# Kernel tuning notes

Hardware: AMD Instinct MI355X
Metric: run time of the kernel (lower is better)

The kernel has to match this reference:

```python
import jax, jax.numpy as jnp
import numpy as np

B = 32768      # batch
D = 512        # embedding dim
V = 100000     # vocab_length (row 0 reserved -> table has V+1 rows)
S = 100        # num_neg_samples (hard-coded in source)
DISTORTION = 0.4


def _expected_counts():
    # fixed_unigram sampler: zipf-ish counts, distorted by 0.4, 1 reserved id
    counts = 1.0 / np.arange(1, V + 1, dtype=np.float64)
    p = counts ** DISTORTION
    p = p / p.sum()
    q = np.zeros(V + 1, dtype=np.float64)
    # unique sampling expected count: E[id in sample] = 1-(1-p)^S
    q[1:] = -np.expm1(S * np.log1p(-p))
    q[0] = 1e-9  # reserved id, never sampled; avoid log(0)
    return q


def setup_inputs() -> dict:
    key = jax.random.key(0)
    k1, k2, k3, k4 = jax.random.split(key, 4)
    label = jax.random.randint(k1, (B,), 1, V + 1, dtype=jnp.int64)
    inputs = jax.random.normal(k2, (B, D), dtype=jnp.float32)
    weights = jax.random.normal(k3, (V + 1, D), dtype=jnp.float32) * 0.05
    biases = jnp.zeros((V + 1,), dtype=jnp.float32)
    sampled_ids = jax.random.choice(k4, V, (S,), replace=False).astype(jnp.int64) + 1
    q = jnp.asarray(_expected_counts(), dtype=jnp.float32)
    true_expected_count = q[label]          # [B]
    sampled_expected_count = q[sampled_ids]  # [S]
    return {
        "label": label, "inputs": inputs, "weights": weights, "biases": biases,
        "sampled_ids": sampled_ids,
        "true_expected_count": true_expected_count,
        "sampled_expected_count": sampled_expected_count,
    }


def reference(label, inputs, weights, biases, sampled_ids,
              true_expected_count, sampled_expected_count):
    # --- _compute_sampled_logits with subtract_log_q=True ---
    true_w = weights[label]                                   # [B, D] gather
    true_logits = (jnp.einsum('bd,bd->b', inputs, true_w)
                   + biases[label]
                   - jnp.log(true_expected_count))            # [B]
    samp_w = weights[sampled_ids]                             # [S, D] gather
    samp_logits = (jnp.einsum('bd,sd->bs', inputs, samp_w)
                   + biases[sampled_ids]
                   - jnp.log(sampled_expected_count))         # [B, S]
    logits = jnp.concatenate([true_logits[:, None], samp_logits], axis=1)  # [B, 1+S]
    # labels are one-hot at column 0 -> CE = logsumexp - true logit
    losses = jax.nn.logsumexp(logits, axis=1) - logits[:, 0]
    loss = jnp.mean(losses)
    return logits, loss
```

## Files before the change

kernel.cpp:

```cpp
#include <hip/hip_runtime.h>
#include <math.h>

#define B_TOT 32768
#define DIM   512
#define NS    100
#define NCOL  101
#define TB    128
#define NBLK  (B_TOT / TB)

#define BASE_OFF 28672
#define LPART_OFF 28800
#define NPACK (16 * 7 * 64)

typedef __attribute__((ext_vector_type(8))) short short8;
typedef __attribute__((ext_vector_type(4))) float f32x4;

static __device__ __forceinline__ short f2bf(float f) {
    unsigned u = __builtin_bit_cast(unsigned, f);
    unsigned r = (u + 0x7FFFu + ((u >> 16) & 1u)) >> 16;
    return (short)r;
}

__global__ __launch_bounds__(256)
void pack_kernel(const float* __restrict__ weights, const float* __restrict__ biases,
                 const int* __restrict__ sids, const float* __restrict__ sq,
                 short* __restrict__ wpack, float* __restrict__ base_g)
{
    const int tid = blockIdx.x * 256 + threadIdx.x;
    if (tid < 112)
        base_g[tid] = (tid < NS) ? biases[sids[tid]] - logf(sq[tid]) : -INFINITY;
    if (tid >= NPACK) return;
    const int kc = tid / 448, rem = tid % 448;
    const int c = rem >> 6, l = rem & 63;
    const int col = c * 16 + (l & 15);
    const int k   = kc * 32 + (l >> 4) * 8;
    short8 v = (short8){0, 0, 0, 0, 0, 0, 0, 0};
    if (col < NS) {
        const float* src = weights + (long)sids[col] * DIM + k;
        const float4 f0 = *(const float4*)src;
        const float4 f1 = *(const float4*)(src + 4);
        v[0] = f2bf(f0.x); v[1] = f2bf(f0.y); v[2] = f2bf(f0.z); v[3] = f2bf(f0.w);
        v[4] = f2bf(f1.x); v[5] = f2bf(f1.y); v[6] = f2bf(f1.z); v[7] = f2bf(f1.w);
    }
    *(short8*)&wpack[(long)tid * 8] = v;
}

__global__ __launch_bounds__(512, 4)
void fused_kernel(const int* __restrict__ label,
                  const float* __restrict__ inputs,
                  const float* __restrict__ weights,
                  const float* __restrict__ biases,
                  const float* __restrict__ tq,
                  const short* __restrict__ wpack,
                  const float* __restrict__ base_g,
                  float* __restrict__ out,
                  float* __restrict__ lpart)
{
    const int t    = threadIdx.x;
    const int wave = t >> 6;
    const int lane = t & 63;
    const int rit  = lane & 15;
    const int seg  = lane >> 4;
    const int absRow = blockIdx.x * TB + wave * 16 + rit;
    const int lab = label[absRow];
    const float* aptr = inputs  + (long)absRow * DIM + seg * 8;
    const float* wtp  = weights + (long)lab    * DIM + seg * 8;

    float base_v[7];
    #pragma unroll
    for (int c = 0; c < 7; c++) base_v[c] = base_g[c * 16 + rit];

    f32x4 acc[7];
    #pragma unroll
    for (int c = 0; c < 7; c++) acc[c] = (f32x4){0.f, 0.f, 0.f, 0.f};
    float tacc = 0.f;

    #pragma unroll
    for (int kc = 0; kc < DIM / 32; kc++) {
        const int k0 = kc * 32;
        const float4 a0 = *(const float4*)(aptr + k0);
        const float4 a1 = *(const float4*)(aptr + k0 + 4);
        const float4 w0 = *(const float4*)(wtp + k0);
        const float4 w1 = *(const float4*)(wtp + k0 + 4);

        tacc = fmaf(a0.x, w0.x, tacc); tacc = fmaf(a0.y, w0.y, tacc);
        tacc = fmaf(a0.z, w0.z, tacc); tacc = fmaf(a0.w, w0.w, tacc);
        tacc = fmaf(a1.x, w1.x, tacc); tacc = fmaf(a1.y, w1.y, tacc);
        tacc = fmaf(a1.z, w1.z, tacc); tacc = fmaf(a1.w, w1.w, tacc);

        short8 af;
        af[0] = f2bf(a0.x); af[1] = f2bf(a0.y); af[2] = f2bf(a0.z); af[3] = f2bf(a0.w);
        af[4] = f2bf(a1.x); af[5] = f2bf(a1.y); af[6] = f2bf(a1.z); af[7] = f2bf(a1.w);

        const short* wp = wpack + ((long)kc * 7 * 64 + lane) * 8;
        #pragma unroll
        for (int c = 0; c < 7; c++) {
            const short8 bf = *(const short8*)(wp + c * 64 * 8);
            acc[c] = __builtin_amdgcn_mfma_f32_16x16x32_bf16(af, bf, acc[c], 0, 0, 0);
        }
    }

    tacc += __shfl_xor(tacc, 16);
    tacc += __shfl_xor(tacc, 32);
    const float tl = tacc + biases[lab] - logf(tq[absRow]);
    if (lane < 16) out[(long)absRow * NCOL] = tl;

    const int g = lane >> 4;
    float loss_sum = 0.f;
    #pragma unroll
    for (int i = 0; i < 4; i++) {
        const int r = g * 4 + i;
        const long orow = (long)(blockIdx.x * TB + wave * 16 + r) * NCOL;
        const float tlv = __shfl(tl, r);
        float v[7];
        float m = tlv;
        #pragma unroll
        for (int c = 0; c < 7; c++) {
            v[c] = acc[c][i] + base_v[c];
            m = fmaxf(m, v[c]);
        }
        #pragma unroll
        for (int off = 1; off < 16; off <<= 1) m = fmaxf(m, __shfl_xor(m, off));
        float s = (rit == 0) ? expf(tlv - m) : 0.f;
        #pragma unroll
        for (int c = 0; c < 7; c++) s += expf(v[c] - m);
        #pragma unroll
        for (int off = 1; off < 16; off <<= 1) s += __shfl_xor(s, off);
        loss_sum += m + logf(s) - tlv;
        #pragma unroll
        for (int c = 0; c < 7; c++) {
            const int col = c * 16 + rit;
            if (col < NS) out[orow + 1 + col] = v[c];
        }
    }
    float wl = (rit == 0) ? loss_sum : 0.f;
    wl += __shfl_xor(wl, 16);
    wl += __shfl_xor(wl, 32);
    if (lane == 0) lpart[blockIdx.x * 8 + wave] = wl;
}

__global__ __launch_bounds__(256)
void reduce_kernel(const float* __restrict__ lpart, float* __restrict__ out_loss)
{
    double s = 0.0;
    for (int i = threadIdx.x; i < NBLK * 8; i += 256) s += (double)lpart[i];
    __shared__ double buf[256];
    buf[threadIdx.x] = s;
    __syncthreads();
    for (int o = 128; o > 0; o >>= 1) {
        if (threadIdx.x < o) buf[threadIdx.x] += buf[threadIdx.x + o];
        __syncthreads();
    }
    if (threadIdx.x == 0) *out_loss = (float)(buf[0] * (1.0 / (double)B_TOT));
}

extern "C" void kernel_launch(void* const* d_in, const int* in_sizes, int n_in,
                              void* d_out, int out_size, void* d_ws, size_t ws_size,
                              hipStream_t stream)
{
    const int*   label   = (const int*)d_in[0];
    const float* inputs  = (const float*)d_in[1];
    const float* weights = (const float*)d_in[2];
    const float* biases  = (const float*)d_in[3];
    const int*   sids    = (const int*)d_in[4];
    const float* tq      = (const float*)d_in[5];
    const float* sq      = (const float*)d_in[6];
    float* out  = (float*)d_out;
    float* ws_f = (float*)d_ws;
    short* wpack  = (short*)d_ws;
    float* base_g = ws_f + BASE_OFF;
    float* lpart  = ws_f + LPART_OFF;

    pack_kernel<<<28, 256, 0, stream>>>(weights, biases, sids, sq, wpack, base_g);
    fused_kernel<<<NBLK, 512, 0, stream>>>(label, inputs, weights, biases, tq,
                                           wpack, base_g, out, lpart);
    reduce_kernel<<<1, 256, 0, stream>>>(lpart, out + (long)B_TOT * NCOL);
}
```

Before: 44.02 us.

## Stage packed weights in LDS and split K across wave pairs

The fused kernel now launches 1024 threads per block. It copies the whole bf16 packed sample-weight matrix (about 112 KB) into LDS once per block, and pairs of waves each handle half of the K dimension for the same 16 rows. Their partial MFMA accumulators and true-logit dot products are combined through LDS before the softmax/loss epilogue. The aim is to cut repeated global/L2 reads of the packed weights and double the wave parallelism per row tile. In exchange, the large LDS footprint likely limits residency to one block per CU, and the change adds extra barriers and an LDS reduction step. The per-block loss is also pre-summed, so the reduce kernel reads only 256 values.

New measurement: 41.40 us. -5.9%, faster.

```diff
diff --git a/kernel.cpp b/kernel.cpp
--- a/kernel.cpp
+++ b/kernel.cpp
@@ -7,10 +7,10 @@
 #define NCOL  101
 #define TB    128
 #define NBLK  (B_TOT / TB)
+#define NPACK (16 * 7 * 64)
 
 #define BASE_OFF 28672
 #define LPART_OFF 28800
-#define NPACK (16 * 7 * 64)
 
 typedef __attribute__((ext_vector_type(8))) short short8;
 typedef __attribute__((ext_vector_type(4))) float f32x4;
@@ -45,7 +45,7 @@
     *(short8*)&wpack[(long)tid * 8] = v;
 }
 
-__global__ __launch_bounds__(512, 4)
+__global__ __launch_bounds__(1024, 4)
 void fused_kernel(const int* __restrict__ label,
                   const float* __restrict__ inputs,
                   const float* __restrict__ weights,
@@ -56,27 +56,40 @@
                   float* __restrict__ out,
                   float* __restrict__ lpart)
 {
-    const int t    = threadIdx.x;
+    __shared__ short W_lds[NPACK * 8];
+    __shared__ float tl_x[TB];
+    __shared__ float ls_lds[8];
+
+    const int t = threadIdx.x;
+
+    {
+        const short8* src = (const short8*)wpack;
+        short8* dst = (short8*)W_lds;
+        #pragma unroll
+        for (int s = 0; s < 7; s++)
+            dst[s * 1024 + t] = src[s * 1024 + t];
+    }
+
     const int wave = t >> 6;
     const int lane = t & 63;
+    const int rg   = wave >> 1;
+    const int kh   = wave & 1;
     const int rit  = lane & 15;
     const int seg  = lane >> 4;
-    const int absRow = blockIdx.x * TB + wave * 16 + rit;
+    const int absRow = blockIdx.x * TB + rg * 16 + rit;
     const int lab = label[absRow];
-    const float* aptr = inputs  + (long)absRow * DIM + seg * 8;
-    const float* wtp  = weights + (long)lab    * DIM + seg * 8;
-
-    float base_v[7];
-    #pragma unroll
-    for (int c = 0; c < 7; c++) base_v[c] = base_g[c * 16 + rit];
+    const float* aptr = inputs  + (long)absRow * DIM + kh * 256 + seg * 8;
+    const float* wtp  = weights + (long)lab    * DIM + kh * 256 + seg * 8;
 
     f32x4 acc[7];
     #pragma unroll
     for (int c = 0; c < 7; c++) acc[c] = (f32x4){0.f, 0.f, 0.f, 0.f};
     float tacc = 0.f;
 
+    __syncthreads();
+
     #pragma unroll
-    for (int kc = 0; kc < DIM / 32; kc++) {
+    for (int kc = 0; kc < 8; kc++) {
         const int k0 = kc * 32;
         const float4 a0 = *(const float4*)(aptr + k0);
         const float4 a1 = *(const float4*)(aptr + k0 + 4);
@@ -92,7 +105,8 @@
         af[0] = f2bf(a0.x); af[1] = f2bf(a0.y); af[2] = f2bf(a0.z); af[3] = f2bf(a0.w);
         af[4] = f2bf(a1.x); af[5] = f2bf(a1.y); af[6] = f2bf(a1.z); af[7] = f2bf(a1.w);
 
-        const short* wp = wpack + ((long)kc * 7 * 64 + lane) * 8;
+        const int kcg = kh * 8 + kc;
+        const short* wp = &W_lds[((kcg * 7) * 64 + lane) * 8];
         #pragma unroll
         for (int c = 0; c < 7; c++) {
             const short8 bf = *(const short8*)(wp + c * 64 * 8);
@@ -102,50 +116,84 @@
 
     tacc += __shfl_xor(tacc, 16);
     tacc += __shfl_xor(tacc, 32);
-    const float tl = tacc + biases[lab] - logf(tq[absRow]);
-    if (lane < 16) out[(long)absRow * NCOL] = tl;
-
-    const int g = lane >> 4;
-    float loss_sum = 0.f;
-    #pragma unroll
-    for (int i = 0; i < 4; i++) {
-        const int r = g * 4 + i;
-        const long orow = (long)(blockIdx.x * TB + wave * 16 + r) * NCOL;
-        const float tlv = __shfl(tl, r);
-        float v[7];
-        float m = tlv;
-        #pragma unroll
-        for (int c = 0; c < 7; c++) {
-            v[c] = acc[c][i] + base_v[c];
-            m = fmaxf(m, v[c]);
+
+    __syncthreads();
+
+    float* ex = (float*)W_lds;
+    if (kh == 1) {
+        const int base = rg * 1856 + lane * 29;
+        #pragma unroll
+        for (int c = 0; c < 7; c++)
+            #pragma unroll
+            for (int i = 0; i < 4; i++)
+                ex[base + c * 4 + i] = acc[c][i];
+        if (lane < 16) tl_x[rg * 16 + lane] = tacc;
+    }
+    __syncthreads();
+
+    if (kh == 0) {
+        const int base = rg * 1856 + lane * 29;
+        #pragma unroll
+        for (int c = 0; c < 7; c++)
+            #pragma unroll
+            for (int i = 0; i < 4; i++)
+                acc[c][i] += ex[base + c * 4 + i];
+        tacc += tl_x[rg * 16 + rit];
+
+        float base_v[7];
+        #pragma unroll
+        for (int c = 0; c < 7; c++) base_v[c] = base_g[c * 16 + rit];
+
+        const float tl = tacc + biases[lab] - logf(tq[absRow]);
+        if (lane < 16) out[(long)absRow * NCOL] = tl;
+
+        const int g = lane >> 4;
+        float loss_sum = 0.f;
+        #pragma unroll
+        for (int i = 0; i < 4; i++) {
+            const int r = g * 4 + i;
+            const long orow = (long)(blockIdx.x * TB + rg * 16 + r) * NCOL;
+            const float tlv = __shfl(tl, r);
+            float v[7];
+            float m = tlv;
+            #pragma unroll
+            for (int c = 0; c < 7; c++) {
+                v[c] = acc[c][i] + base_v[c];
+                m = fmaxf(m, v[c]);
+            }
+            #pragma unroll
+            for (int off = 1; off < 16; off <<= 1) m = fmaxf(m, __shfl_xor(m, off));
+            float s = (rit == 0) ? expf(tlv - m) : 0.f;
+            #pragma unroll
+            for (int c = 0; c < 7; c++) s += expf(v[c] - m);
+            #pragma unroll
+            for (int off = 1; off < 16; off <<= 1) s += __shfl_xor(s, off);
+            loss_sum += m + logf(s) - tlv;
+            #pragma unroll
+            for (int c = 0; c < 7; c++) {
+                const int col = c * 16 + rit;
+                if (col < NS) out[orow + 1 + col] = v[c];
+            }
         }
-        #pragma unroll
-        for (int off = 1; off < 16; off <<= 1) m = fmaxf(m, __shfl_xor(m, off));
-        float s = (rit == 0) ? expf(tlv - m) : 0.f;
-        #pragma unroll
-        for (int c = 0; c < 7; c++) s += expf(v[c] - m);
-        #pragma unroll
-        for (int off = 1; off < 16; off <<= 1) s += __shfl_xor(s, off);
-        loss_sum += m + logf(s) - tlv;
-        #pragma unroll
-        for (int c = 0; c < 7; c++) {
-            const int col = c * 16 + rit;
-            if (col < NS) out[orow + 1 + col] = v[c];
-        }
-    }
-    float wl = (rit == 0) ? loss_sum : 0.f;
-    wl += __shfl_xor(wl, 16);
-    wl += __shfl_xor(wl, 32);
-    if (lane == 0) lpart[blockIdx.x * 8 + wave] = wl;
+        float wl = (rit == 0) ? loss_sum : 0.f;
+        wl += __shfl_xor(wl, 16);
+        wl += __shfl_xor(wl, 32);
+        if (lane == 0) ls_lds[rg] = wl;
+    }
+    __syncthreads();
+    if (t == 0) {
+        float bp = 0.f;
+        #pragma unroll
+        for (int w = 0; w < 8; w++) bp += ls_lds[w];
+        lpart[blockIdx.x] = bp;
+    }
 }
 
 __global__ __launch_bounds__(256)
 void reduce_kernel(const float* __restrict__ lpart, float* __restrict__ out_loss)
 {
-    double s = 0.0;
-    for (int i = threadIdx.x; i < NBLK * 8; i += 256) s += (double)lpart[i];
     __shared__ double buf[256];
-    buf[threadIdx.x] = s;
+    buf[threadIdx.x] = (double)lpart[threadIdx.x];
     __syncthreads();
     for (int o = 128; o > 0; o >>= 1) {
         if (threadIdx.x < o) buf[threadIdx.x] += buf[threadIdx.x + o];
@@ -172,7 +220,7 @@
     float* lpart  = ws_f + LPART_OFF;
 
     pack_kernel<<<28, 256, 0, stream>>>(weights, biases, sids, sq, wpack, base_g);
-    fused_kernel<<<NBLK, 512, 0, stream>>>(label, inputs, weights, biases, tq,
-                                           wpack, base_g, out, lpart);
+    fused_kernel<<<NBLK, 1024, 0, stream>>>(label, inputs, weights, biases, tq,
+                                            wpack, base_g, out, lpart);
     reduce_kernel<<<1, 256, 0, stream>>>(lpart, out + (long)B_TOT * NCOL);
 }
```
